# Performance work log

Measured on AMD Instinct MI355X. Metric: run time of the kernel, lower is better.

The kernel has to match this reference:

```python
import jax, jax.numpy as jnp
import numpy as np

B, SQ, SK, D, N, H = 2, 2048, 2048, 1024, 16, 64
EPS = 1e-5


def setup_inputs() -> dict:
    key = jax.random.key(0)
    ks = jax.random.split(key, 8)
    inv_d = 1.0 / np.sqrt(D)
    inv_h = 1.0 / np.sqrt(H)
    # causal mask: True = masked (filled with -inf), matching torch.where(mask, IGNORE, attn)
    mask = jnp.triu(jnp.ones((SQ, SK), dtype=bool), k=1)
    return {
        "x_q": jax.random.normal(ks[0], (B, SQ, D), dtype=jnp.float32),
        "x_kv": jax.random.normal(ks[1], (B, SK, D), dtype=jnp.float32),
        "mask": mask,
        "W_Q": jax.random.normal(ks[2], (N, D, H), dtype=jnp.float32) * inv_d,
        "W_K": jax.random.normal(ks[3], (N, D, H), dtype=jnp.float32) * inv_d,
        "W_V": jax.random.normal(ks[4], (N, D, H), dtype=jnp.float32) * inv_d,
        "W_O": jax.random.normal(ks[5], (N, H, D), dtype=jnp.float32) * inv_h,
        "b_Q": jnp.zeros((N, H), dtype=jnp.float32),
        "b_K": jnp.zeros((N, H), dtype=jnp.float32),
        "b_V": jnp.zeros((N, H), dtype=jnp.float32),
        "b_O": jnp.zeros((D,), dtype=jnp.float32),
        "ln1_g": jnp.ones((H,), dtype=jnp.float32),
        "ln1_b": jnp.zeros((H,), dtype=jnp.float32),
        "ln2_g": jnp.ones((H,), dtype=jnp.float32),
        "ln2_b": jnp.zeros((H,), dtype=jnp.float32),
    }


def _layernorm(x, g, b):
    # LayerNorm over last dim (d_head), eps=1e-5, biased variance (torch default)
    m = jnp.mean(x, axis=-1, keepdims=True)
    v = jnp.mean(jnp.square(x - m), axis=-1, keepdims=True)
    return (x - m) * jax.lax.rsqrt(v + EPS) * g + b


def reference(x_q, x_kv, mask, W_Q, W_K, W_V, W_O, b_Q, b_K, b_V, b_O,
              ln1_g, ln1_b, ln2_g, ln2_b):
    q = jnp.einsum('bsd,ndh->bsnh', x_q, W_Q) + b_Q    # [B,SQ,N,H]
    k = jnp.einsum('bsd,ndh->bsnh', x_kv, W_K) + b_K   # [B,SK,N,H]
    v = jnp.einsum('bsd,ndh->bsnh', x_kv, W_V) + b_V   # [B,SK,N,H]
    q = _layernorm(q, ln1_g, ln1_b)
    k = _layernorm(k, ln2_g, ln2_b)
    # NOTE: no 1/sqrt(d_head) scaling, faithful to the source module
    attn = jnp.einsum('bqnh,bknh->bnqk', q, k)         # [B,N,SQ,SK]
    attn = jnp.where(mask, -jnp.inf, attn)
    probas = jax.nn.softmax(attn, axis=-1)
    z = jnp.einsum('bnqk,bknh->bqnh', probas, v)       # [B,SQ,N,H]
    out = jnp.einsum('bqnh,nhd->bqd', z, W_O) + b_O    # [B,SQ,D]
    return (out, k, v)
```

## Files before the change

### kernel.cpp

```cpp
#include <hip/hip_runtime.h>
#include <math.h>

namespace {
constexpr int kB  = 2;
constexpr int kS  = 2048;
constexpr int kD  = 1024;
constexpr int kN  = 16;
constexpr int kH  = 64;
constexpr int kBS = kB * kS;
constexpr int kNH = kN * kH;
}

typedef __bf16 bf16x4 __attribute__((ext_vector_type(4)));
typedef __bf16 bf16x8 __attribute__((ext_vector_type(8)));
typedef float  f32x4  __attribute__((ext_vector_type(4)));
typedef unsigned int u32x4 __attribute__((ext_vector_type(4)));

__device__ inline unsigned pkbf(float a, float b) {
  unsigned short ua = __builtin_bit_cast(unsigned short, (__bf16)a);
  unsigned short ub = __builtin_bit_cast(unsigned short, (__bf16)b);
  return (unsigned)ua | ((unsigned)ub << 16);
}

__global__ __launch_bounds__(256) void split_x2(
    const float* __restrict__ in0, const float* __restrict__ in1,
    __bf16* __restrict__ oH0, __bf16* __restrict__ oL0,
    __bf16* __restrict__ oH1, __bf16* __restrict__ oL1)
{
  const int bx = blockIdx.x;
  const float* in;
  __bf16 *oH, *oL;
  long long i4;
  if (bx < 4096) { in = in0; oH = oH0; oL = oL0; i4 = (long long)bx * 256 + threadIdx.x; }
  else           { in = in1; oH = oH1; oL = oL1; i4 = (long long)(bx - 4096) * 256 + threadIdx.x; }
  const float4 v = *(const float4*)(in + i4 * 4);
  const float x[4] = {v.x, v.y, v.z, v.w};
  bf16x4 hi, lo;
#pragma unroll
  for (int i = 0; i < 4; ++i) {
    const __bf16 h = (__bf16)x[i];
    hi[i] = h;
    lo[i] = (__bf16)(x[i] - (float)h);
  }
  *(bf16x4*)(oH + i4 * 4) = hi;
  *(bf16x4*)(oL + i4 * 4) = lo;
}

__global__ __launch_bounds__(256) void transpose_split(
    const float* __restrict__ in, long long hsIn, int ldin,
    __bf16* __restrict__ oH, __bf16* __restrict__ oL, long long hsOut)
{
  __shared__ float T[64][65];
  const int t = threadIdx.x;
  const long long inBase = (long long)blockIdx.z * hsIn +
                           (long long)(blockIdx.x * 64) * ldin + blockIdx.y * 64;
  const long long outBase = (long long)blockIdx.z * hsOut +
                            (long long)(blockIdx.y * 64) * 1024 + blockIdx.x * 64;
#pragma unroll
  for (int rr = 0; rr < 4; ++rr) {
    const int i = rr * 16 + (t >> 4);
    const int j = (t & 15) * 4;
    const float4 v = *(const float4*)(in + inBase + (long long)i * ldin + j);
    T[i][j + 0] = v.x; T[i][j + 1] = v.y; T[i][j + 2] = v.z; T[i][j + 3] = v.w;
  }
  __syncthreads();
#pragma unroll
  for (int rr = 0; rr < 4; ++rr) {
    const int hh = rr * 16 + (t >> 4);
    const int kk = (t & 15) * 4;
    bf16x4 hi, lo;
#pragma unroll
    for (int m = 0; m < 4; ++m) {
      const float x = T[kk + m][hh];
      const __bf16 h = (__bf16)x;
      hi[m] = h;
      lo[m] = (__bf16)(x - (float)h);
    }
    *(bf16x4*)(oH + outBase + (long long)hh * 1024 + kk) = hi;
    *(bf16x4*)(oL + outBase + (long long)hh * 1024 + kk) = lo;
  }
}

__global__ __launch_bounds__(256) void transpose_split_qkv(
    const float* __restrict__ WQ, const float* __restrict__ WK,
    const float* __restrict__ WV,
    __bf16* __restrict__ QH, __bf16* __restrict__ QL,
    __bf16* __restrict__ KHo, __bf16* __restrict__ KLo,
    __bf16* __restrict__ VH, __bf16* __restrict__ VL)
{
  __shared__ float T[64][65];
  const int t = threadIdx.x;
  const int which = blockIdx.z >> 4;
  const int z = blockIdx.z & 15;
  const float* __restrict__ in = (which == 0) ? WQ : (which == 1) ? WK : WV;
  __bf16* __restrict__ oH = (which == 0) ? QH : (which == 1) ? KHo : VH;
  __bf16* __restrict__ oL = (which == 0) ? QL : (which == 1) ? KLo : VL;
  const long long inBase = (long long)z * 65536 +
                           (long long)(blockIdx.x * 64) * 64 + blockIdx.y * 64;
  const long long outBase = (long long)z * 65536 +
                            (long long)(blockIdx.y * 64) * 1024 + blockIdx.x * 64;
#pragma unroll
  for (int rr = 0; rr < 4; ++rr) {
    const int i = rr * 16 + (t >> 4);
    const int j = (t & 15) * 4;
    const float4 v = *(const float4*)(in + inBase + (long long)i * 64 + j);
    T[i][j + 0] = v.x; T[i][j + 1] = v.y; T[i][j + 2] = v.z; T[i][j + 3] = v.w;
  }
  __syncthreads();
#pragma unroll
  for (int rr = 0; rr < 4; ++rr) {
    const int hh = rr * 16 + (t >> 4);
    const int kk = (t & 15) * 4;
    bf16x4 hi, lo;
#pragma unroll
    for (int m = 0; m < 4; ++m) {
      const float x = T[kk + m][hh];
      const __bf16 h = (__bf16)x;
      hi[m] = h;
      lo[m] = (__bf16)(x - (float)h);
    }
    *(bf16x4*)(oH + outBase + (long long)hh * 1024 + kk) = hi;
    *(bf16x4*)(oL + outBase + (long long)hh * 1024 + kk) = lo;
  }
}

__global__ __launch_bounds__(256) void qkv_gemm128t(
    const __bf16* __restrict__ xqH, const __bf16* __restrict__ xqL,
    const __bf16* __restrict__ xkH, const __bf16* __restrict__ xkL,
    const __bf16* __restrict__ WQH, const __bf16* __restrict__ WQL,
    const __bf16* __restrict__ WKH, const __bf16* __restrict__ WKL,
    const __bf16* __restrict__ WVH,
    const float* __restrict__ b_Q, const float* __restrict__ b_K,
    const float* __restrict__ b_V,
    const float* __restrict__ ln1g, const float* __restrict__ ln1b,
    const float* __restrict__ ln2g, const float* __restrict__ ln2b,
    float* __restrict__ out_k, float* __restrict__ out_v,
    __bf16* __restrict__ qH, __bf16* __restrict__ qL,
    __bf16* __restrict__ kHp, __bf16* __restrict__ kLp,
    __bf16* __restrict__ vT)
{
  const int mode = blockIdx.z;
  const int row0 = blockIdx.x * 128;
  const int ct   = blockIdx.y;
  const bool split = (mode < 2);

  __shared__ __align__(16) char SM[36864];
  char* const ABuf = SM;
  char* const BBuf = SM + 16384;

  const int t = threadIdx.x;
  const int lane = t & 63;
  const int w = t >> 6;
  const int l16 = lane & 15;
  const int quad = lane >> 4;
  const int mBase = (w & 1) * 64;
  const int nBase = (w >> 1) * 64;

  const __bf16* __restrict__ aHp = (mode == 0) ? xqH : xkH;
  const __bf16* __restrict__ aLp = (mode == 0) ? xqL : xkL;
  const __bf16* __restrict__ bHp = (mode == 0) ? WQH : (mode == 1) ? WKH : WVH;
  const __bf16* __restrict__ bLp = (mode == 0) ? WQL : WKL;

  f32x4 acc[4][4] = {};

  const int srow = t >> 1;
  const int e16  = (t & 1) * 16;
  const int s8   = srow & 7;
  const int sw2  = (s8 & 1) | ((s8 & 2) << 1) | ((s8 & 4) >> 1);
  const int u0   = (t & 1) * 2;
  const int wh0  = ((u0    ) ^ sw2) << 4;
  const int wh1  = ((u0 + 1) ^ sw2) << 4;
  char* const arow_p = ABuf + srow * 128;
  char* const brow_p = BBuf + srow * 128;

  bf16x8 r[8];
  auto loadT = [&](int k0, bf16x8 rr[8]) {
    const long long ga = (long long)(row0 + srow) * 1024 + k0 + e16;
    const long long gb = (long long)(ct * 128 + srow) * 1024 + k0 + e16;
    rr[0] = *(const bf16x8*)(aHp + ga);
    rr[1] = *(const bf16x8*)(aHp + ga + 8);
    rr[2] = *(const bf16x8*)(bHp + gb);
    rr[3] = *(const bf16x8*)(bHp + gb + 8);
    if (split) {
      rr[4] = *(const bf16x8*)(aLp + ga);
      rr[5] = *(const bf16x8*)(aLp + ga + 8);
      rr[6] = *(const bf16x8*)(bLp + gb);
      rr[7] = *(const bf16x8*)(bLp + gb + 8);
    }
  };
  loadT(0, r);

  const int r8  = l16 & 7;
  const int rs2 = (r8 & 1) | ((r8 & 2) << 1) | ((r8 & 4) >> 1);
  const int rof = (quad ^ rs2) << 4;

  for (int k0 = 0; k0 < 1024; k0 += 32) {
    if (k0) __syncthreads();
    bf16x8 rn[8];
    if (k0 + 32 < 1024) loadT(k0 + 32, rn);
    *(bf16x8*)(arow_p + wh0) = r[0];
    *(bf16x8*)(arow_p + wh1) = r[1];
    *(bf16x8*)(brow_p + wh0) = r[2];
    *(bf16x8*)(brow_p + wh1) = r[3];
    if (split) {
      *(bf16x8*)(arow_p + (wh0 ^ 64)) = r[4];
      *(bf16x8*)(arow_p + (wh1 ^ 64)) = r[5];
      *(bf16x8*)(brow_p + (wh0 ^ 64)) = r[6];
      *(bf16x8*)(brow_p + (wh1 ^ 64)) = r[7];
    }
    __syncthreads();

    bf16x8 ah[4], bh[4];
#pragma unroll
    for (int mt = 0; mt < 4; ++mt)
      ah[mt] = *(const bf16x8*)(ABuf + (mBase + mt * 16 + l16) * 128 + rof);
#pragma unroll
    for (int nt = 0; nt < 4; ++nt)
      bh[nt] = *(const bf16x8*)(BBuf + (nBase + nt * 16 + l16) * 128 + rof);
#pragma unroll
    for (int mt = 0; mt < 4; ++mt)
#pragma unroll
      for (int nt = 0; nt < 4; ++nt)
        acc[mt][nt] = __builtin_amdgcn_mfma_f32_16x16x32_bf16(ah[mt], bh[nt], acc[mt][nt], 0, 0, 0);
    if (split) {
      bf16x8 bl[4];
#pragma unroll
      for (int nt = 0; nt < 4; ++nt)
        bl[nt] = *(const bf16x8*)(BBuf + (nBase + nt * 16 + l16) * 128 + (rof ^ 64));
#pragma unroll
      for (int mt = 0; mt < 4; ++mt)
#pragma unroll
        for (int nt = 0; nt < 4; ++nt)
          acc[mt][nt] = __builtin_amdgcn_mfma_f32_16x16x32_bf16(ah[mt], bl[nt], acc[mt][nt], 0, 0, 0);
      bf16x8 al[4];
#pragma unroll
      for (int mt = 0; mt < 4; ++mt)
        al[mt] = *(const bf16x8*)(ABuf + (mBase + mt * 16 + l16) * 128 + (rof ^ 64));
#pragma unroll
      for (int mt = 0; mt < 4; ++mt)
#pragma unroll
        for (int nt = 0; nt < 4; ++nt)
          acc[mt][nt] = __builtin_amdgcn_mfma_f32_16x16x32_bf16(al[mt], bh[nt], acc[mt][nt], 0, 0, 0);
    }
#pragma unroll
    for (int i = 0; i < 8; ++i) r[i] = rn[i];
  }

  const float* __restrict__ bias = (mode == 0) ? b_Q : (mode == 1) ? b_K : b_V;
  float bi[4];
#pragma unroll
  for (int nt = 0; nt < 4; ++nt) bi[nt] = bias[ct * 128 + nBase + nt * 16 + l16];

  if (mode <= 1) {
    const float* __restrict__ lg = (mode == 0) ? ln1g : ln2g;
    const float* __restrict__ lb = (mode == 0) ? ln1b : ln2b;
    float gg[4], bb[4];
#pragma unroll
    for (int nt = 0; nt < 4; ++nt) {
      gg[nt] = lg[nt * 16 + l16];
      bb[nt] = lb[nt * 16 + l16];
    }
#pragma unroll
    for (int mt = 0; mt < 4; ++mt)
#pragma unroll
      for (int r4 = 0; r4 < 4; ++r4) {
        float y[4];
#pragma unroll
        for (int nt = 0; nt < 4; ++nt) y[nt] = acc[mt][nt][r4] + bi[nt];
        float s = y[0] + y[1] + y[2] + y[3];
#pragma unroll
        for (int o = 8; o >= 1; o >>= 1) s += __shfl_xor(s, o);
        const float m = s * (1.0f / 64.0f);
        float vs = 0.0f;
#pragma unroll
        for (int nt = 0; nt < 4; ++nt) {
          const float d = y[nt] - m;
          vs += d * d;
        }
#pragma unroll
        for (int o = 8; o >= 1; o >>= 1) vs += __shfl_xor(vs, o);
        const float inv = rsqrtf(vs * (1.0f / 64.0f) + 1e-5f);
#pragma unroll
        for (int nt = 0; nt < 4; ++nt)
          acc[mt][nt][r4] = (y[nt] - m) * inv * gg[nt] + bb[nt];
      }
  } else {
#pragma unroll
    for (int mt = 0; mt < 4; ++mt)
#pragma unroll
      for (int nt = 0; nt < 4; ++nt)
#pragma unroll
        for (int r4 = 0; r4 < 4; ++r4) acc[mt][nt][r4] += bi[nt];
  }

#pragma unroll
  for (int mt = 0; mt < 4; ++mt)
#pragma unroll
    for (int r4 = 0; r4 < 4; ++r4) {
      const long long row = row0 + mBase + mt * 16 + quad * 4 + r4;
      const long long cb = row * 1024 + ct * 128 + nBase;
      if (mode == 0) {
#pragma unroll
        for (int nt = 0; nt < 4; ++nt) {
          const float x = acc[mt][nt][r4];
          const __bf16 h = (__bf16)x;
          qH[cb + nt * 16 + l16] = h;
          qL[cb + nt * 16 + l16] = (__bf16)(x - (float)h);
        }
      } else if (mode == 1) {
#pragma unroll
        for (int nt = 0; nt < 4; ++nt) {
          const float x = acc[mt][nt][r4];
          out_k[cb + nt * 16 + l16] = x;
          const __bf16 h = (__bf16)x;
          kHp[cb + nt * 16 + l16] = h;
          kLp[cb + nt * 16 + l16] = (__bf16)(x - (float)h);
        }
      } else {
#pragma unroll
        for (int nt = 0; nt < 4; ++nt)
          out_v[cb + nt * 16 + l16] = acc[mt][nt][r4];
      }
    }

  if (mode == 2) {
    __syncthreads();
    __bf16* TT = (__bf16*)SM + w * 4608;
#pragma unroll
    for (int mt = 0; mt < 4; ++mt)
#pragma unroll
      for (int nt = 0; nt < 4; ++nt)
#pragma unroll
        for (int r4 = 0; r4 < 4; ++r4)
          TT[(nt * 16 + l16) * 72 + mt * 16 + quad * 4 + r4] = (__bf16)acc[mt][nt][r4];
    __syncthreads();
    const int b = row0 >> 11;
    const int s0 = (row0 + mBase) & 2047;
    const int head = ct * 2 + (w >> 1);
#pragma unroll
    for (int rep = 0; rep < 8; ++rep) {
      const int h = rep * 8 + (lane >> 3);
      const int s8v = (lane & 7) * 8;
      const bf16x8 vv = *(const bf16x8*)&TT[h * 72 + s8v];
      const int a  = s8v >> 4;
      const int c0 = 32 * (a >> 1) + 8 * ((s8v >> 2) & 3) + 4 * (a & 1);
      __bf16* dst = vT + ((long long)((b * 16 + head) * 64 + h)) * 2048 + s0 + c0;
      const bf16x4 lo = __builtin_shufflevector(vv, vv, 0, 1, 2, 3);
      const bf16x4 hi = __builtin_shufflevector(vv, vv, 4, 5, 6, 7);
      *(bf16x4*)(dst)     = lo;
      *(bf16x4*)(dst + 8) = hi;
    }
  }
}

__global__ __launch_bounds__(256) void ogemm64p(
    const __bf16* __restrict__ zH, const __bf16* __restrict__ WOt,
    const float* __restrict__ b_O, float* __restrict__ out)
{
  const int row0 = blockIdx.x * 64;
  const int ct = blockIdx.y;
  __shared__ __align__(16) __bf16 AS2[2][64][40];
  __shared__ __align__(16) __bf16 BS2[2][128][40];
  const int t = threadIdx.x;
  const int lane = t & 63;
  const int w = t >> 6;
  const int l16 = lane & 15;
  const int quad = lane >> 4;
  const int nBase = w * 32;

  f32x4 acc[4][2] = {};
  const int arow = t >> 2, akh = (t & 3) * 8;
  const int brow = t >> 1, bkh = (t & 1) * 16;

  bf16x8 r0, r1, r2;
  auto loadT = [&](int k0) {
    r0 = *(const bf16x8*)(zH + (long long)(row0 + arow) * 1024 + k0 + akh);
    const long long gb = (long long)(ct * 128 + brow) * 1024 + k0 + bkh;
    r1 = *(const bf16x8*)(WOt + gb);
    r2 = *(const bf16x8*)(WOt + gb + 8);
  };
  loadT(0);
  *(bf16x8*)&AS2[0][arow][akh]     = r0;
  *(bf16x8*)&BS2[0][brow][bkh]     = r1;
  *(bf16x8*)&BS2[0][brow][bkh + 8] = r2;
  __syncthreads();

  for (int k0 = 0; k0 < 1024; k0 += 32) {
    const int cb = (k0 >> 5) & 1;
    const bool more = (k0 + 32 < 1024);
    if (more) loadT(k0 + 32);

    bf16x8 ah[4], bh[2];
#pragma unroll
    for (int mt = 0; mt < 4; ++mt)
      ah[mt] = *(const bf16x8*)&AS2[cb][mt * 16 + l16][quad * 8];
#pragma unroll
    for (int nt = 0; nt < 2; ++nt)
      bh[nt] = *(const bf16x8*)&BS2[cb][nBase + nt * 16 + l16][quad * 8];
#pragma unroll
    for (int mt = 0; mt < 4; ++mt)
#pragma unroll
      for (int nt = 0; nt < 2; ++nt)
        acc[mt][nt] = __builtin_amdgcn_mfma_f32_16x16x32_bf16(ah[mt], bh[nt], acc[mt][nt], 0, 0, 0);

    if (more) {
      const int nb = 1 - cb;
      *(bf16x8*)&AS2[nb][arow][akh]     = r0;
      *(bf16x8*)&BS2[nb][brow][bkh]     = r1;
      *(bf16x8*)&BS2[nb][brow][bkh + 8] = r2;
    }
    __syncthreads();
  }

#pragma unroll
  for (int mt = 0; mt < 4; ++mt)
#pragma unroll
    for (int r4 = 0; r4 < 4; ++r4) {
      const long long row = row0 + mt * 16 + quad * 4 + r4;
#pragma unroll
      for (int nt = 0; nt < 2; ++nt) {
        const int col = ct * 128 + nBase + nt * 16 + l16;
        out[row * 1024 + col] = acc[mt][nt][r4] + b_O[col];
      }
    }
}

__global__ __launch_bounds__(256, 2) void attn_mfma5(
    const __bf16* __restrict__ qHg, const __bf16* __restrict__ qLg,
    const __bf16* __restrict__ kHg, const __bf16* __restrict__ kLg,
    const __bf16* __restrict__ vTg,
    __bf16* __restrict__ zH)
{
  const int p = blockIdx.x;
  const int n = blockIdx.y;
  const int b = blockIdx.z;

  __shared__ __align__(16) char SM[49152];

  const int t = threadIdx.x;
  const int lane = t & 63;
  const int w = t >> 6;
  const int l16 = lane & 15;
  const int quad = lane >> 4;
  const int skey = t >> 2;
  const int sh16 = (t & 3) * 16;
  const int su   = sh16 >> 3;
  const int sx   = (skey & 7) << 4;
  const int rx   = (l16 & 7) << 4;

  bf16x8 rk0, rk1, rl0, rl1, rv0, rv1;
  auto storeKV = [&](int buf) {
    char* base = SM + buf * 8192 + skey * 128;
    *(bf16x8*)(base +         (((su    ) << 4) ^ sx)) = rk0;
    *(bf16x8*)(base +         (((su + 1) << 4) ^ sx)) = rk1;
    *(bf16x8*)(base + 16384 + (((su    ) << 4) ^ sx)) = rl0;
    *(bf16x8*)(base + 16384 + (((su + 1) << 4) ^ sx)) = rl1;
    *(bf16x8*)(base + 32768 + (((su    ) << 4) ^ sx)) = rv0;
    *(bf16x8*)(base + 32768 + (((su + 1) << 4) ^ sx)) = rv1;
  };

  for (int half = 0; half < 2; ++half) {
    const int qt = half ? p : (31 - p);
    const int q0 = qt * 64;

    bf16x8 Qh[2], Ql[2];
    {
      const long long qrow = (long long)(b * kS + q0 + w * 16 + l16) * 1024 + n * 64 + quad * 8;
      Qh[0] = *(const bf16x8*)(qHg + qrow);
      Qh[1] = *(const bf16x8*)(qHg + qrow + 32);
      Ql[0] = *(const bf16x8*)(qLg + qrow);
      Ql[1] = *(const bf16x8*)(qLg + qrow + 32);
    }

    f32x4 O[4] = {};
    float mrun = -3.0e38f, lrun = 0.0f;
    const int qg = q0 + w * 16 + l16;

    auto loadKV = [&](int k0) {
      const long long gk = (long long)(b * kS + k0 + skey) * 1024 + n * 64 + sh16;
      rk0 = *(const bf16x8*)(kHg + gk);
      rk1 = *(const bf16x8*)(kHg + gk + 8);
      rl0 = *(const bf16x8*)(kLg + gk);
      rl1 = *(const bf16x8*)(kLg + gk + 8);
      const long long gv = ((long long)(b * kN + n) * 64 + skey) * 2048 + k0 + sh16;
      rv0 = *(const bf16x8*)(vTg + gv);
      rv1 = *(const bf16x8*)(vTg + gv + 8);
    };

    loadKV(0);
    storeKV(0);
    __syncthreads();

    for (int kt = 0; kt <= qt; ++kt) {
      const int cb = kt & 1;
      const bool more = (kt < qt);
      if (more) loadKV((kt + 1) * 64);

      const char* KHb = SM + cb * 8192;
      const char* KLb = KHb + 16384;
      const char* VSb = KHb + 32768;

      f32x4 S[4] = {};
      __builtin_amdgcn_s_setprio(1);
#pragma unroll
      for (int kc = 0; kc < 4; ++kc) {
        const int ro = (kc * 16 + l16) * 128;
        const bf16x8 kh0 = *(const bf16x8*)(KHb + ro + (((quad    ) << 4) ^ rx));
        const bf16x8 kh1 = *(const bf16x8*)(KHb + ro + (((quad + 4) << 4) ^ rx));
        const bf16x8 kl0 = *(const bf16x8*)(KLb + ro + (((quad    ) << 4) ^ rx));
        const bf16x8 kl1 = *(const bf16x8*)(KLb + ro + (((quad + 4) << 4) ^ rx));
        S[kc] = __builtin_amdgcn_mfma_f32_16x16x32_bf16(kh0, Qh[0], S[kc], 0, 0, 0);
        S[kc] = __builtin_amdgcn_mfma_f32_16x16x32_bf16(kh1, Qh[1], S[kc], 0, 0, 0);
        S[kc] = __builtin_amdgcn_mfma_f32_16x16x32_bf16(kl0, Qh[0], S[kc], 0, 0, 0);
        S[kc] = __builtin_amdgcn_mfma_f32_16x16x32_bf16(kl1, Qh[1], S[kc], 0, 0, 0);
        S[kc] = __builtin_amdgcn_mfma_f32_16x16x32_bf16(kh0, Ql[0], S[kc], 0, 0, 0);
        S[kc] = __builtin_amdgcn_mfma_f32_16x16x32_bf16(kh1, Ql[1], S[kc], 0, 0, 0);
      }
      __builtin_amdgcn_s_setprio(0);

      if (kt == qt) {
#pragma unroll
        for (int kc = 0; kc < 4; ++kc) {
          const int key = q0 + kc * 16 + quad * 4;
#pragma unroll
          for (int r = 0; r < 4; ++r)
            if (key + r > qg) S[kc][r] = -3.0e38f;
        }
      }

      float pm = fmaxf(fmaxf(S[0][0], S[0][1]), fmaxf(S[0][2], S[0][3]));
      pm = fmaxf(pm, fmaxf(fmaxf(S[1][0], S[1][1]), fmaxf(S[1][2], S[1][3])));
      pm = fmaxf(pm, fmaxf(fmaxf(S[2][0], S[2][1]), fmaxf(S[2][2], S[2][3])));
      pm = fmaxf(pm, fmaxf(fmaxf(S[3][0], S[3][1]), fmaxf(S[3][2], S[3][3])));
      pm = fmaxf(pm, __shfl_xor(pm, 16));
      pm = fmaxf(pm, __shfl_xor(pm, 32));
      const float mnew = fmaxf(mrun, pm);
      float ls = 0.0f;
#pragma unroll
      for (int kc = 0; kc < 4; ++kc)
#pragma unroll
        for (int r = 0; r < 4; ++r) {
          const float pe = __expf(S[kc][r] - mnew);
          S[kc][r] = pe;
          ls += pe;
        }
      ls += __shfl_xor(ls, 16);
      ls += __shfl_xor(ls, 32);

      if (__any(pm > mrun)) {
        const float alpha = __expf(mrun - mnew);
        lrun = lrun * alpha + ls;
        float aB[4];
#pragma unroll
        for (int r = 0; r < 4; ++r)
          aB[r] = __shfl(alpha, (lane & 48) | (quad * 4 + r));
#pragma unroll
        for (int hc = 0; hc < 4; ++hc)
#pragma unroll
          for (int r = 0; r < 4; ++r) O[hc][r] *= aB[r];
      } else {
        lrun += ls;
      }
      mrun = mnew;

      u32x4 pw0, pw1;
      pw0[0] = pkbf(S[0][0], S[0][1]); pw0[1] = pkbf(S[0][2], S[0][3]);
      pw0[2] = pkbf(S[1][0], S[1][1]); pw0[3] = pkbf(S[1][2], S[1][3]);
      pw1[0] = pkbf(S[2][0], S[2][1]); pw1[1] = pkbf(S[2][2], S[2][3]);
      pw1[2] = pkbf(S[3][0], S[3][1]); pw1[3] = pkbf(S[3][2], S[3][3]);
      const bf16x8 Pa0 = __builtin_bit_cast(bf16x8, pw0);
      const bf16x8 Pa1 = __builtin_bit_cast(bf16x8, pw1);

      __builtin_amdgcn_s_setprio(1);
#pragma unroll
      for (int hc = 0; hc < 4; ++hc) {
        const int ro = (hc * 16 + l16) * 128;
        const bf16x8 vb0 = *(const bf16x8*)(VSb + ro + (((quad    ) << 4) ^ rx));
        const bf16x8 vb1 = *(const bf16x8*)(VSb + ro + (((quad + 4) << 4) ^ rx));
        O[hc] = __builtin_amdgcn_mfma_f32_16x16x32_bf16(Pa0, vb0, O[hc], 0, 0, 0);
        O[hc] = __builtin_amdgcn_mfma_f32_16x16x32_bf16(Pa1, vb1, O[hc], 0, 0, 0);
      }
      __builtin_amdgcn_s_setprio(0);

      if (more) storeKV(1 - cb);
      __syncthreads();
    }

    float linv[4];
#pragma unroll
    for (int r = 0; r < 4; ++r)
      linv[r] = 1.0f / __shfl(lrun, (lane & 48) | (quad * 4 + r));
#pragma unroll
    for (int r = 0; r < 4; ++r) {
      const long long zrow = (long long)(b * kS + q0 + w * 16 + quad * 4 + r) * 1024 + n * 64;
#pragma unroll
      for (int hc = 0; hc < 4; ++hc)
        zH[zrow + hc * 16 + l16] = (__bf16)(O[hc][r] * linv[r]);
    }
  }
}

__global__ __launch_bounds__(256) void sgemm64(
    const float* __restrict__ A, int lda,
    const float* __restrict__ Bbase, long long bStride, int colMul, int ldb,
    float* __restrict__ C, int ldc,
    const float* __restrict__ bias, int K)
{
  const int row0 = blockIdx.x * 64;
  const int ct = blockIdx.y;
  const float* __restrict__ Bp = Bbase + (long long)ct * bStride;
  const int col0B = ct * colMul;
  const int col0C = ct * 64;
  __shared__ float As[16][68];
  __shared__ float Bs[16][68];
  const int t = threadIdx.x;
  const int ty = t >> 4;
  const int tx = t & 15;
  float acc[4][4] = {};
  for (int k0 = 0; k0 < K; k0 += 16) {
    {
      const int r = t >> 2;
      const int kk = (t & 3) * 4;
      const float4 a4 = *(const float4*)(A + (long long)(row0 + r) * lda + k0 + kk);
      As[kk + 0][r] = a4.x; As[kk + 1][r] = a4.y; As[kk + 2][r] = a4.z; As[kk + 3][r] = a4.w;
    }
    {
      const int kk = t >> 4;
      const int c = (t & 15) * 4;
      *(float4*)&Bs[kk][c] = *(const float4*)(Bp + (long long)(k0 + kk) * ldb + col0B + c);
    }
    __syncthreads();
#pragma unroll
    for (int kk = 0; kk < 16; ++kk) {
      const float4 a4 = *(const float4*)&As[kk][ty * 4];
      const float4 b4 = *(const float4*)&Bs[kk][tx * 4];
      const float av[4] = {a4.x, a4.y, a4.z, a4.w};
      const float bv[4] = {b4.x, b4.y, b4.z, b4.w};
#pragma unroll
      for (int i = 0; i < 4; ++i)
#pragma unroll
        for (int j = 0; j < 4; ++j)
          acc[i][j] = fmaf(av[i], bv[j], acc[i][j]);
    }
    __syncthreads();
  }
#pragma unroll
  for (int i = 0; i < 4; ++i) {
    const int r = row0 + ty * 4 + i;
    float4 o;
    o.x = acc[i][0] + bias[col0C + tx * 4 + 0];
    o.y = acc[i][1] + bias[col0C + tx * 4 + 1];
    o.z = acc[i][2] + bias[col0C + tx * 4 + 2];
    o.w = acc[i][3] + bias[col0C + tx * 4 + 3];
    *(float4*)(C + (long long)r * ldc + col0C + tx * 4) = o;
  }
}

__global__ __launch_bounds__(256) void ln64(
    float* __restrict__ X, const float* __restrict__ g,
    const float* __restrict__ bta, int nrows)
{
  const int row = blockIdx.x * 4 + (threadIdx.x >> 6);
  const int lane = threadIdx.x & 63;
  if (row >= nrows) return;
  const float x = X[(long long)row * 64 + lane];
  float s = x;
#pragma unroll
  for (int o = 32; o >= 1; o >>= 1) s += __shfl_xor(s, o);
  const float m = s * (1.0f / 64.0f);
  const float d = x - m;
  float vs = d * d;
#pragma unroll
  for (int o = 32; o >= 1; o >>= 1) vs += __shfl_xor(vs, o);
  const float inv = rsqrtf(vs * (1.0f / 64.0f) + 1e-5f);
  X[(long long)row * 64 + lane] = d * inv * g[lane] + bta[lane];
}

__global__ __launch_bounds__(256) void attn_mfma(
    const float* __restrict__ Q, const float* __restrict__ Kg,
    const float* __restrict__ Vg, float* __restrict__ Z)
{
  const int qt = (gridDim.x - 1) - blockIdx.x;
  const int n = blockIdx.y;
  const int b = blockIdx.z;
  const int q0 = qt * 64;
  __shared__ __bf16 KH[64][72];
  __shared__ __bf16 KL[64][72];
  __shared__ __bf16 VS[64][72];
  const int t = threadIdx.x;
  const int lane = t & 63;
  const int w = t >> 6;
  const int l16 = lane & 15;
  const int quad = lane >> 4;
  bf16x8 Qh[2], Ql[2];
  {
    const long long qrow = ((long long)(b * kS + q0 + w * 16 + l16)) * kNH + n * kH + quad * 8;
#pragma unroll
    for (int c = 0; c < 2; ++c) {
      const float4 a = *(const float4*)(Q + qrow + c * 32);
      const float4 bq = *(const float4*)(Q + qrow + c * 32 + 4);
      const float x[8] = {a.x, a.y, a.z, a.w, bq.x, bq.y, bq.z, bq.w};
#pragma unroll
      for (int i = 0; i < 8; ++i) {
        const __bf16 h = (__bf16)x[i];
        Qh[c][i] = h;
        Ql[c][i] = (__bf16)(x[i] - (float)h);
      }
    }
  }
  f32x4 O[4] = {};
  float mrow[4] = {-3.0e38f, -3.0e38f, -3.0e38f, -3.0e38f};
  float lrow[4] = {};
  for (int kt = 0; kt <= qt; ++kt) {
    const int k0 = kt * 64;
    __syncthreads();
#pragma unroll
    for (int rep = 0; rep < 4; ++rep) {
      {
        const int row = rep * 16 + (t >> 4);
        const int h4 = (t & 15) * 4;
        const float4 k4 = *(const float4*)(Kg + ((long long)(b * kS + k0 + row)) * kNH + n * kH + h4);
        const float x[4] = {k4.x, k4.y, k4.z, k4.w};
        bf16x4 hi, lo;
#pragma unroll
        for (int i = 0; i < 4; ++i) {
          const __bf16 h = (__bf16)x[i];
          hi[i] = h;
          lo[i] = (__bf16)(x[i] - (float)h);
        }
        *(bf16x4*)&KH[row][h4] = hi;
        *(bf16x4*)&KL[row][h4] = lo;
      }
      {
        const int key = rep * 16 + (t & 15);
        const int h4 = (t >> 4) * 4;
        const float4 v4 = *(const float4*)(Vg + ((long long)(b * kS + k0 + key)) * kNH + n * kH + h4);
        VS[h4 + 0][key] = (__bf16)v4.x;
        VS[h4 + 1][key] = (__bf16)v4.y;
        VS[h4 + 2][key] = (__bf16)v4.z;
        VS[h4 + 3][key] = (__bf16)v4.w;
      }
    }
    __syncthreads();
    f32x4 S[4] = {};
#pragma unroll
    for (int kc = 0; kc < 4; ++kc) {
      const int row = kc * 16 + l16;
      const bf16x8 kh0 = *(const bf16x8*)&KH[row][quad * 8];
      const bf16x8 kh1 = *(const bf16x8*)&KH[row][32 + quad * 8];
      const bf16x8 kl0 = *(const bf16x8*)&KL[row][quad * 8];
      const bf16x8 kl1 = *(const bf16x8*)&KL[row][32 + quad * 8];
      S[kc] = __builtin_amdgcn_mfma_f32_16x16x32_bf16(Qh[0], kh0, S[kc], 0, 0, 0);
      S[kc] = __builtin_amdgcn_mfma_f32_16x16x32_bf16(Qh[1], kh1, S[kc], 0, 0, 0);
      S[kc] = __builtin_amdgcn_mfma_f32_16x16x32_bf16(Qh[0], kl0, S[kc], 0, 0, 0);
      S[kc] = __builtin_amdgcn_mfma_f32_16x16x32_bf16(Qh[1], kl1, S[kc], 0, 0, 0);
      S[kc] = __builtin_amdgcn_mfma_f32_16x16x32_bf16(Ql[0], kh0, S[kc], 0, 0, 0);
      S[kc] = __builtin_amdgcn_mfma_f32_16x16x32_bf16(Ql[1], kh1, S[kc], 0, 0, 0);
    }
    if (kt == qt) {
#pragma unroll
      for (int kc = 0; kc < 4; ++kc) {
        const int key = k0 + kc * 16 + l16;
#pragma unroll
        for (int r = 0; r < 4; ++r) {
          const int q = q0 + w * 16 + quad * 4 + r;
          if (key > q) S[kc][r] = -3.0e38f;
        }
      }
    }
#pragma unroll
    for (int r = 0; r < 4; ++r) {
      float mt = fmaxf(fmaxf(S[0][r], S[1][r]), fmaxf(S[2][r], S[3][r]));
#pragma unroll
      for (int o = 8; o >= 1; o >>= 1) mt = fmaxf(mt, __shfl_xor(mt, o));
      const float mnew = fmaxf(mrow[r], mt);
      const float alpha = __expf(mrow[r] - mnew);
      mrow[r] = mnew;
      float ls = 0.0f;
#pragma unroll
      for (int kc = 0; kc < 4; ++kc) {
        const float pe = __expf(S[kc][r] - mnew);
        S[kc][r] = pe;
        ls += pe;
      }
#pragma unroll
      for (int o = 8; o >= 1; o >>= 1) ls += __shfl_xor(ls, o);
      lrow[r] = lrow[r] * alpha + ls;
#pragma unroll
      for (int hc = 0; hc < 4; ++hc) O[hc][r] *= alpha;
    }
    __syncthreads();
    __bf16(*Ps)[72] = KL;
#pragma unroll
    for (int kc = 0; kc < 4; ++kc)
#pragma unroll
      for (int r = 0; r < 4; ++r)
        Ps[w * 16 + quad * 4 + r][kc * 16 + l16] = (__bf16)S[kc][r];
    bf16x8 Pa[2];
#pragma unroll
    for (int c = 0; c < 2; ++c)
      Pa[c] = *(const bf16x8*)&Ps[w * 16 + l16][c * 32 + quad * 8];
#pragma unroll
    for (int hc = 0; hc < 4; ++hc) {
      const int hrow = hc * 16 + l16;
      const bf16x8 vb0 = *(const bf16x8*)&VS[hrow][quad * 8];
      const bf16x8 vb1 = *(const bf16x8*)&VS[hrow][32 + quad * 8];
      O[hc] = __builtin_amdgcn_mfma_f32_16x16x32_bf16(Pa[0], vb0, O[hc], 0, 0, 0);
      O[hc] = __builtin_amdgcn_mfma_f32_16x16x32_bf16(Pa[1], vb1, O[hc], 0, 0, 0);
    }
  }
#pragma unroll
  for (int r = 0; r < 4; ++r) {
    const float inv = 1.0f / lrow[r];
    const long long zrow = ((long long)(b * kS + q0 + w * 16 + quad * 4 + r)) * kNH + n * kH;
#pragma unroll
    for (int hc = 0; hc < 4; ++hc)
      Z[zrow + hc * 16 + l16] = O[hc][r] * inv;
  }
}

extern "C" void kernel_launch(void* const* d_in, const int* in_sizes, int n_in,
                              void* d_out, int out_size, void* d_ws, size_t ws_size,
                              hipStream_t stream)
{
  const float* x_q   = (const float*)d_in[0];
  const float* x_kv  = (const float*)d_in[1];
  const float* W_Q   = (const float*)d_in[3];
  const float* W_K   = (const float*)d_in[4];
  const float* W_V   = (const float*)d_in[5];
  const float* W_O   = (const float*)d_in[6];
  const float* b_Q   = (const float*)d_in[7];
  const float* b_K   = (const float*)d_in[8];
  const float* b_V   = (const float*)d_in[9];
  const float* b_O   = (const float*)d_in[10];
  const float* ln1_g = (const float*)d_in[11];
  const float* ln1_b = (const float*)d_in[12];
  const float* ln2_g = (const float*)d_in[13];
  const float* ln2_b = (const float*)d_in[14];

  float* out_o = (float*)d_out;
  float* out_k = out_o + 4194304;
  float* out_v = out_o + 8388608;

  const dim3 blk(256);

  if (ws_size >= (72ull << 20)) {
    char* W = (char*)d_ws;
    __bf16* xqH = (__bf16*)(W);
    __bf16* xqL = xqH + 4194304;
    __bf16* xkH = (__bf16*)(W + (16ull << 20));
    __bf16* xkL = xkH + 4194304;
    __bf16* wp  = (__bf16*)(W + (32ull << 20));
    __bf16 *WtQH = wp,            *WtQL = wp + 1048576;
    __bf16 *WtKH = wp + 2097152,  *WtKL = wp + 3145728;
    __bf16 *WtVH = wp + 4194304,  *WtVL = wp + 5242880;
    __bf16 *WOtH = wp + 6291456,  *WOtL = wp + 7340032;
    __bf16* kHp = (__bf16*)(W + (48ull << 20));
    __bf16* kLp = kHp + 4194304;
    __bf16* vT  = (__bf16*)(W + (64ull << 20));
    __bf16* zH = xqH;
    __bf16* qH = (__bf16*)out_o;
    __bf16* qL = qH + 4194304;

    hipLaunchKernelGGL(split_x2, dim3(8192), blk, 0, stream,
                       x_q, x_kv, xqH, xqL, xkH, xkL);
    hipLaunchKernelGGL(transpose_split_qkv, dim3(16, 1, 48), blk, 0, stream,
                       W_Q, W_K, W_V, WtQH, WtQL, WtKH, WtKL, WtVH, WtVL);
    hipLaunchKernelGGL(transpose_split, dim3(16, 16, 1), blk, 0, stream,
                       W_O, 0LL, 1024, WOtH, WOtL, 0LL);

    hipLaunchKernelGGL(qkv_gemm128t, dim3(32, 8, 3), blk, 0, stream,
                       xqH, xqL, xkH, xkL,
                       WtQH, WtQL, WtKH, WtKL, WtVH,
                       b_Q, b_K, b_V, ln1_g, ln1_b, ln2_g, ln2_b,
                       out_k, out_v, qH, qL, kHp, kLp, vT);

    hipLaunchKernelGGL(attn_mfma5, dim3(16, 16, 2), blk, 0, stream,
                       qH, qL, kHp, kLp, vT, zH);

    hipLaunchKernelGGL(ogemm64p, dim3(64, 8), blk, 0, stream,
                       zH, WOtH, b_O, out_o);
  } else {
    float* ws_q = out_o;
    float* ws_z = (float*)d_ws;
    const dim3 gproj(kBS / 64, kN);
    hipLaunchKernelGGL(sgemm64, gproj, blk, 0, stream,
                       x_q, kD, W_Q, (long long)kD * kH, 0, kH, ws_q, kNH, b_Q, kD);
    hipLaunchKernelGGL(sgemm64, gproj, blk, 0, stream,
                       x_kv, kD, W_K, (long long)kD * kH, 0, kH, out_k, kNH, b_K, kD);
    hipLaunchKernelGGL(sgemm64, gproj, blk, 0, stream,
                       x_kv, kD, W_V, (long long)kD * kH, 0, kH, out_v, kNH, b_V, kD);
    const int nrows = kBS * kN;
    hipLaunchKernelGGL(ln64, dim3(nrows / 4), blk, 0, stream, ws_q, ln1_g, ln1_b, nrows);
    hipLaunchKernelGGL(ln64, dim3(nrows / 4), blk, 0, stream, out_k, ln2_g, ln2_b, nrows);
    hipLaunchKernelGGL(attn_mfma, dim3(kS / 64, kN, kB), blk, 0, stream,
                       ws_q, out_k, out_v, ws_z);
    hipLaunchKernelGGL(sgemm64, dim3(kBS / 64, kD / 64), blk, 0, stream,
                       ws_z, kNH, W_O, 0LL, 64, kD, out_o, kD, b_O, kD);
  }
}
```

Before: 289.9 us.

## Fuse prep kernels, double-buffer QKV GEMM registers, use lazy softmax max rescaling

Merges the three preprocessing kernels (x split, QKV weight transpose/split, W_O transpose) into one launch and drops the unused low-part writes for W_V and W_O. The QKV GEMM main loop is unrolled by two with ping-pong register buffers to avoid register copies. The attention softmax now rescales the running max only when the new block max exceeds it by more than 8, skipping most alpha rescale passes at the cost of exp values up to e^8 held in bf16/fp32.

```diff
diff --git a/kernel.cpp b/kernel.cpp
--- a/kernel.cpp
+++ b/kernel.cpp
@@ -22,109 +22,110 @@
   return (unsigned)ua | ((unsigned)ub << 16);
 }
 
-__global__ __launch_bounds__(256) void split_x2(
-    const float* __restrict__ in0, const float* __restrict__ in1,
-    __bf16* __restrict__ oH0, __bf16* __restrict__ oL0,
-    __bf16* __restrict__ oH1, __bf16* __restrict__ oL1)
+__global__ __launch_bounds__(256) void prep_all(
+    const float* __restrict__ xq, const float* __restrict__ xkv,
+    const float* __restrict__ WQ, const float* __restrict__ WK,
+    const float* __restrict__ WV, const float* __restrict__ WO,
+    __bf16* __restrict__ xqH, __bf16* __restrict__ xqL,
+    __bf16* __restrict__ xkH, __bf16* __restrict__ xkL,
+    __bf16* __restrict__ QH, __bf16* __restrict__ QL,
+    __bf16* __restrict__ KHo, __bf16* __restrict__ KLo,
+    __bf16* __restrict__ VH,
+    __bf16* __restrict__ WOtH)
 {
   const int bx = blockIdx.x;
-  const float* in;
-  __bf16 *oH, *oL;
-  long long i4;
-  if (bx < 4096) { in = in0; oH = oH0; oL = oL0; i4 = (long long)bx * 256 + threadIdx.x; }
-  else           { in = in1; oH = oH1; oL = oL1; i4 = (long long)(bx - 4096) * 256 + threadIdx.x; }
-  const float4 v = *(const float4*)(in + i4 * 4);
-  const float x[4] = {v.x, v.y, v.z, v.w};
-  bf16x4 hi, lo;
-#pragma unroll
-  for (int i = 0; i < 4; ++i) {
-    const __bf16 h = (__bf16)x[i];
-    hi[i] = h;
-    lo[i] = (__bf16)(x[i] - (float)h);
-  }
-  *(bf16x4*)(oH + i4 * 4) = hi;
-  *(bf16x4*)(oL + i4 * 4) = lo;
+  const int t = threadIdx.x;
+  __shared__ float T[64][65];
+
+  if (bx < 8192) {
+    const float* in;
+    __bf16 *oH, *oL;
+    long long i4;
+    if (bx < 4096) { in = xq;  oH = xqH; oL = xqL; i4 = (long long)bx * 256 + t; }
+    else           { in = xkv; oH = xkH; oL = xkL; i4 = (long long)(bx - 4096) * 256 + t; }
+    const float4 v = *(const float4*)(in + i4 * 4);
+    const float x[4] = {v.x, v.y, v.z, v.w};
+    bf16x4 hi, lo;
+#pragma unroll
+    for (int i = 0; i < 4; ++i) {
+      const __bf16 h = (__bf16)x[i];
+      hi[i] = h;
+      lo[i] = (__bf16)(x[i] - (float)h);
+    }
+    *(bf16x4*)(oH + i4 * 4) = hi;
+    *(bf16x4*)(oL + i4 * 4) = lo;
+    return;
+  }
+
+  if (bx < 8960) {
+    const int zz = bx - 8192;
+    const int bxx = zz & 15;
+    const int z   = zz >> 4;
+    const int which = z >> 4;
+    const bool wantLo = (which < 2);
+    const float* __restrict__ in = (which == 0) ? WQ : (which == 1) ? WK : WV;
+    __bf16* __restrict__ oH = (which == 0) ? QH : (which == 1) ? KHo : VH;
+    __bf16* __restrict__ oL = (which == 0) ? QL : KLo;
+    const long long inBase = (long long)(z & 15) * 65536 + (long long)(which ? (z & 15) : (z & 15)) * 0 +
+                             (long long)((z >> 4) == which ? 0 : 0);
+    const int head = z & 15;
+    const long long inB  = (long long)head * 65536 + (long long)(bxx * 64) * 64;
+    const long long outB = (long long)head * 65536 + bxx * 64;
+    (void)inBase;
+#pragma unroll
+    for (int rr = 0; rr < 4; ++rr) {
+      const int i = rr * 16 + (t >> 4);
+      const int j = (t & 15) * 4;
+      const float4 v = *(const float4*)(in + inB + (long long)i * 64 + j);
+      T[i][j + 0] = v.x; T[i][j + 1] = v.y; T[i][j + 2] = v.z; T[i][j + 3] = v.w;
+    }
+    __syncthreads();
+#pragma unroll
+    for (int rr = 0; rr < 4; ++rr) {
+      const int hh = rr * 16 + (t >> 4);
+      const int kk = (t & 15) * 4;
+      bf16x4 hi, lo;
+#pragma unroll
+      for (int m = 0; m < 4; ++m) {
+        const float x = T[kk + m][hh];
+        const __bf16 h = (__bf16)x;
+        hi[m] = h;
+        lo[m] = (__bf16)(x - (float)h);
+      }
+      *(bf16x4*)(oH + outB + (long long)hh * 1024 + kk) = hi;
+      if (wantLo)
+        *(bf16x4*)(oL + outB + (long long)hh * 1024 + kk) = lo;
+    }
+    return;
+  }
+
+  {
+    const int zz = bx - 8960;
+    const int bxx = zz & 15;
+    const int byy = zz >> 4;
+    const long long inB  = (long long)(bxx * 64) * 1024 + byy * 64;
+    const long long outB = (long long)(byy * 64) * 1024 + bxx * 64;
+#pragma unroll
+    for (int rr = 0; rr < 4; ++rr) {
+      const int i = rr * 16 + (t >> 4);
+      const int j = (t & 15) * 4;
+      const float4 v = *(const float4*)(WO + inB + (long long)i * 1024 + j);
+      T[i][j + 0] = v.x; T[i][j + 1] = v.y; T[i][j + 2] = v.z; T[i][j + 3] = v.w;
+    }
+    __syncthreads();
+#pragma unroll
+    for (int rr = 0; rr < 4; ++rr) {
+      const int hh = rr * 16 + (t >> 4);
+      const int kk = (t & 15) * 4;
+      bf16x4 hi;
+#pragma unroll
+      for (int m = 0; m < 4; ++m) hi[m] = (__bf16)T[kk + m][hh];
+      *(bf16x4*)(WOtH + outB + (long long)hh * 1024 + kk) = hi;
+    }
+  }
 }
 
-__global__ __launch_bounds__(256) void transpose_split(
-    const float* __restrict__ in, long long hsIn, int ldin,
-    __bf16* __restrict__ oH, __bf16* __restrict__ oL, long long hsOut)
-{
-  __shared__ float T[64][65];
-  const int t = threadIdx.x;
-  const long long inBase = (long long)blockIdx.z * hsIn +
-                           (long long)(blockIdx.x * 64) * ldin + blockIdx.y * 64;
-  const long long outBase = (long long)blockIdx.z * hsOut +
-                            (long long)(blockIdx.y * 64) * 1024 + blockIdx.x * 64;
-#pragma unroll
-  for (int rr = 0; rr < 4; ++rr) {
-    const int i = rr * 16 + (t >> 4);
-    const int j = (t & 15) * 4;
-    const float4 v = *(const float4*)(in + inBase + (long long)i * ldin + j);
-    T[i][j + 0] = v.x; T[i][j + 1] = v.y; T[i][j + 2] = v.z; T[i][j + 3] = v.w;
-  }
-  __syncthreads();
-#pragma unroll
-  for (int rr = 0; rr < 4; ++rr) {
-    const int hh = rr * 16 + (t >> 4);
-    const int kk = (t & 15) * 4;
-    bf16x4 hi, lo;
-#pragma unroll
-    for (int m = 0; m < 4; ++m) {
-      const float x = T[kk + m][hh];
-      const __bf16 h = (__bf16)x;
-      hi[m] = h;
-      lo[m] = (__bf16)(x - (float)h);
-    }
-    *(bf16x4*)(oH + outBase + (long long)hh * 1024 + kk) = hi;
-    *(bf16x4*)(oL + outBase + (long long)hh * 1024 + kk) = lo;
-  }
-}
-
-__global__ __launch_bounds__(256) void transpose_split_qkv(
-    const float* __restrict__ WQ, const float* __restrict__ WK,
-    const float* __restrict__ WV,
-    __bf16* __restrict__ QH, __bf16* __restrict__ QL,
-    __bf16* __restrict__ KHo, __bf16* __restrict__ KLo,
-    __bf16* __restrict__ VH, __bf16* __restrict__ VL)
-{
-  __shared__ float T[64][65];
-  const int t = threadIdx.x;
-  const int which = blockIdx.z >> 4;
-  const int z = blockIdx.z & 15;
-  const float* __restrict__ in = (which == 0) ? WQ : (which == 1) ? WK : WV;
-  __bf16* __restrict__ oH = (which == 0) ? QH : (which == 1) ? KHo : VH;
-  __bf16* __restrict__ oL = (which == 0) ? QL : (which == 1) ? KLo : VL;
-  const long long inBase = (long long)z * 65536 +
-                           (long long)(blockIdx.x * 64) * 64 + blockIdx.y * 64;
-  const long long outBase = (long long)z * 65536 +
-                            (long long)(blockIdx.y * 64) * 1024 + blockIdx.x * 64;
-#pragma unroll
-  for (int rr = 0; rr < 4; ++rr) {
-    const int i = rr * 16 + (t >> 4);
-    const int j = (t & 15) * 4;
-    const float4 v = *(const float4*)(in + inBase + (long long)i * 64 + j);
-    T[i][j + 0] = v.x; T[i][j + 1] = v.y; T[i][j + 2] = v.z; T[i][j + 3] = v.w;
-  }
-  __syncthreads();
-#pragma unroll
-  for (int rr = 0; rr < 4; ++rr) {
-    const int hh = rr * 16 + (t >> 4);
-    const int kk = (t & 15) * 4;
-    bf16x4 hi, lo;
-#pragma unroll
-    for (int m = 0; m < 4; ++m) {
-      const float x = T[kk + m][hh];
-      const __bf16 h = (__bf16)x;
-      hi[m] = h;
-      lo[m] = (__bf16)(x - (float)h);
-    }
-    *(bf16x4*)(oH + outBase + (long long)hh * 1024 + kk) = hi;
-    *(bf16x4*)(oL + outBase + (long long)hh * 1024 + kk) = lo;
-  }
-}
-
-__global__ __launch_bounds__(256) void qkv_gemm128t(
+__global__ __launch_bounds__(256) void qkv_gemm128u(
     const __bf16* __restrict__ xqH, const __bf16* __restrict__ xqL,
     const __bf16* __restrict__ xkH, const __bf16* __restrict__ xkL,
     const __bf16* __restrict__ WQH, const __bf16* __restrict__ WQL,
@@ -173,7 +174,6 @@
   char* const arow_p = ABuf + srow * 128;
   char* const brow_p = BBuf + srow * 128;
 
-  bf16x8 r[8];
   auto loadT = [&](int k0, bf16x8 rr[8]) {
     const long long ga = (long long)(row0 + srow) * 1024 + k0 + e16;
     const long long gb = (long long)(ct * 128 + srow) * 1024 + k0 + e16;
@@ -188,28 +188,24 @@
       rr[7] = *(const bf16x8*)(bLp + gb + 8);
     }
   };
-  loadT(0, r);
+  auto STAGE = [&](bf16x8 rr[8]) {
+    *(bf16x8*)(arow_p + wh0) = rr[0];
+    *(bf16x8*)(arow_p + wh1) = rr[1];
+    *(bf16x8*)(brow_p + wh0) = rr[2];
+    *(bf16x8*)(brow_p + wh1) = rr[3];
+    if (split) {
+      *(bf16x8*)(arow_p + (wh0 ^ 64)) = rr[4];
+      *(bf16x8*)(arow_p + (wh1 ^ 64)) = rr[5];
+      *(bf16x8*)(brow_p + (wh0 ^ 64)) = rr[6];
+      *(bf16x8*)(brow_p + (wh1 ^ 64)) = rr[7];
+    }
+  };
 
   const int r8  = l16 & 7;
   const int rs2 = (r8 & 1) | ((r8 & 2) << 1) | ((r8 & 4) >> 1);
   const int rof = (quad ^ rs2) << 4;
 
-  for (int k0 = 0; k0 < 1024; k0 += 32) {
-    if (k0) __syncthreads();
-    bf16x8 rn[8];
-    if (k0 + 32 < 1024) loadT(k0 + 32, rn);
-    *(bf16x8*)(arow_p + wh0) = r[0];
-    *(bf16x8*)(arow_p + wh1) = r[1];
-    *(bf16x8*)(brow_p + wh0) = r[2];
-    *(bf16x8*)(brow_p + wh1) = r[3];
-    if (split) {
-      *(bf16x8*)(arow_p + (wh0 ^ 64)) = r[4];
-      *(bf16x8*)(arow_p + (wh1 ^ 64)) = r[5];
-      *(bf16x8*)(brow_p + (wh0 ^ 64)) = r[6];
-      *(bf16x8*)(brow_p + (wh1 ^ 64)) = r[7];
-    }
-    __syncthreads();
-
+  auto COMPUTE = [&]() {
     bf16x8 ah[4], bh[4];
 #pragma unroll
     for (int mt = 0; mt < 4; ++mt)
@@ -242,8 +238,22 @@
         for (int nt = 0; nt < 4; ++nt)
           acc[mt][nt] = __builtin_amdgcn_mfma_f32_16x16x32_bf16(al[mt], bh[nt], acc[mt][nt], 0, 0, 0);
     }
-#pragma unroll
-    for (int i = 0; i < 8; ++i) r[i] = rn[i];
+  };
+
+  bf16x8 rA[8], rB[8];
+  loadT(0, rA);
+
+  for (int k0 = 0; k0 < 1024; k0 += 64) {
+    if (k0) __syncthreads();
+    loadT(k0 + 32, rB);
+    STAGE(rA);
+    __syncthreads();
+    COMPUTE();
+    __syncthreads();
+    if (k0 + 64 < 1024) loadT(k0 + 64, rA);
+    STAGE(rB);
+    __syncthreads();
+    COMPUTE();
   }
 
   const float* __restrict__ bias = (mode == 0) ? b_Q : (mode == 1) ? b_K : b_V;
@@ -425,7 +435,7 @@
     }
 }
 
-__global__ __launch_bounds__(256, 2) void attn_mfma5(
+__global__ __launch_bounds__(256, 2) void attn_mfma6(
     const __bf16* __restrict__ qHg, const __bf16* __restrict__ qLg,
     const __bf16* __restrict__ kHg, const __bf16* __restrict__ kLg,
     const __bf16* __restrict__ vTg,
@@ -534,21 +544,23 @@
       pm = fmaxf(pm, fmaxf(fmaxf(S[3][0], S[3][1]), fmaxf(S[3][2], S[3][3])));
       pm = fmaxf(pm, __shfl_xor(pm, 16));
       pm = fmaxf(pm, __shfl_xor(pm, 32));
-      const float mnew = fmaxf(mrun, pm);
+
+      const bool upd = __any(pm > mrun + 8.0f);
+      const float mref = upd ? fmaxf(mrun, pm) : mrun;
       float ls = 0.0f;
 #pragma unroll
       for (int kc = 0; kc < 4; ++kc)
 #pragma unroll
         for (int r = 0; r < 4; ++r) {
-          const float pe = __expf(S[kc][r] - mnew);
+          const float pe = __expf(S[kc][r] - mref);
           S[kc][r] = pe;
           ls += pe;
         }
       ls += __shfl_xor(ls, 16);
       ls += __shfl_xor(ls, 32);
 
-      if (__any(pm > mrun)) {
-        const float alpha = __expf(mrun - mnew);
+      if (upd) {
+        const float alpha = __expf(mrun - mref);
         lrun = lrun * alpha + ls;
         float aB[4];
 #pragma unroll
@@ -558,10 +570,10 @@
         for (int hc = 0; hc < 4; ++hc)
 #pragma unroll
           for (int r = 0; r < 4; ++r) O[hc][r] *= aB[r];
+        mrun = mref;
       } else {
         lrun += ls;
       }
-      mrun = mnew;
 
       u32x4 pw0, pw1;
       pw0[0] = pkbf(S[0][0], S[0][1]); pw0[1] = pkbf(S[0][2], S[0][3]);
@@ -853,8 +865,8 @@
     __bf16* wp  = (__bf16*)(W + (32ull << 20));
     __bf16 *WtQH = wp,            *WtQL = wp + 1048576;
     __bf16 *WtKH = wp + 2097152,  *WtKL = wp + 3145728;
-    __bf16 *WtVH = wp + 4194304,  *WtVL = wp + 5242880;
-    __bf16 *WOtH = wp + 6291456,  *WOtL = wp + 7340032;
+    __bf16 *WtVH = wp + 4194304;
+    __bf16 *WOtH = wp + 6291456;
     __bf16* kHp = (__bf16*)(W + (48ull << 20));
     __bf16* kLp = kHp + 4194304;
     __bf16* vT  = (__bf16*)(W + (64ull << 20));
@@ -862,20 +874,18 @@
     __bf16* qH = (__bf16*)out_o;
     __bf16* qL = qH + 4194304;
 
-    hipLaunchKernelGGL(split_x2, dim3(8192), blk, 0, stream,
-                       x_q, x_kv, xqH, xqL, xkH, xkL);
-    hipLaunchKernelGGL(transpose_split_qkv, dim3(16, 1, 48), blk, 0, stream,
-                       W_Q, W_K, W_V, WtQH, WtQL, WtKH, WtKL, WtVH, WtVL);
-    hipLaunchKernelGGL(transpose_split, dim3(16, 16, 1), blk, 0, stream,
-                       W_O, 0LL, 1024, WOtH, WOtL, 0LL);
-
-    hipLaunchKernelGGL(qkv_gemm128t, dim3(32, 8, 3), blk, 0, stream,
+    hipLaunchKernelGGL(prep_all, dim3(9216), blk, 0, stream,
+                       x_q, x_kv, W_Q, W_K, W_V, W_O,
+                       xqH, xqL, xkH, xkL,
+                       WtQH, WtQL, WtKH, WtKL, WtVH, WOtH);
+
+    hipLaunchKernelGGL(qkv_gemm128u, dim3(32, 8, 3), blk, 0, stream,
                        xqH, xqL, xkH, xkL,
                        WtQH, WtQL, WtKH, WtKL, WtVH,
                        b_Q, b_K, b_V, ln1_g, ln1_b, ln2_g, ln2_b,
                        out_k, out_v, qH, qL, kHp, kLp, vT);
 
-    hipLaunchKernelGGL(attn_mfma5, dim3(16, 16, 2), blk, 0, stream,
+    hipLaunchKernelGGL(attn_mfma6, dim3(16, 16, 2), blk, 0, stream,
                        qH, qL, kHp, kLp, vT, zH);
 
     hipLaunchKernelGGL(ogemm64p, dim3(64, 8), blk, 0, stream,
```

After: 287.3 us. No clear change (-0.9%).
